# Optimization experiments

Hardware: AMD Instinct MI355X
Metric: run time of the kernel (lower is better)

Reference implementation:

```python
import jax, jax.numpy as jnp
import numpy as np

N = 100000        # num nodes
F_IN = 256        # params['topo_feature']
C = 128           # params['num_edge'] (hidden & GCN channels)
E = 1_600_000     # num edges (avg degree 16)


def setup_inputs() -> dict:
    key = jax.random.key(0)
    k = jax.random.split(key, 6)
    x = jax.random.normal(k[0], (N, F_IN), dtype=jnp.float32)
    edge_index = jax.random.randint(k[1], (2, E), 0, N, dtype=jnp.int32)
    # fc1: Linear(F_IN, C)
    W1 = jax.random.normal(k[2], (C, F_IN), dtype=jnp.float32) * (1.0 / np.sqrt(F_IN))
    b1 = jnp.zeros((C,), dtype=jnp.float32)
    # GCNConv linear: Linear(C, C, bias=False) weight + separate bias added post-aggregation
    W2 = jax.random.normal(k[3], (C, C), dtype=jnp.float32) * (1.0 / np.sqrt(C))
    b2 = jnp.zeros((C,), dtype=jnp.float32)
    return {"x": x, "edge_index": edge_index, "W1": W1, "b1": b1, "W2": W2, "b2": b2}


def reference(x, edge_index, W1, b1, W2, b2):
    # fc1 + relu
    h = jax.nn.relu(x @ W1.T + b1)                       # [N, C]
    # GCNConv: transform, add self-loops, sym-normalize, scatter-add
    z = h @ W2.T                                         # [N, C]
    loop = jnp.arange(N, dtype=edge_index.dtype)
    src = jnp.concatenate([edge_index[0], loop])         # [E+N]
    dst = jnp.concatenate([edge_index[1], loop])         # [E+N]
    deg = jax.ops.segment_sum(jnp.ones_like(dst, jnp.float32), dst, num_segments=N)
    dinv = jnp.where(deg > 0, jax.lax.rsqrt(jnp.maximum(deg, 1.0)), 0.0)
    norm = (dinv[src] * dinv[dst])[:, None]              # [E+N, 1]
    out = jax.ops.segment_sum(z[src] * norm, dst, num_segments=N) + b2
    return out
```

## Files before the change

kernel.cpp:

```cpp
#include <hip/hip_runtime.h>

typedef unsigned short ushort;
typedef __bf16 bf16x8 __attribute__((ext_vector_type(8)));
typedef float f32x4 __attribute__((ext_vector_type(4)));

#define F_IN 256
#define CCH  128
#define BSH  7
#define BNODES 128
#define NBUCK 1024
#define CHUNK 2048

__device__ __forceinline__ ushort f2bf(float f) {
    union { float f; unsigned i; } u; u.f = f;
    unsigned r = u.i + 0x7fffu + ((u.i >> 16) & 1u);
    return (ushort)(r >> 16);
}
__device__ __forceinline__ float2 bf2f2(unsigned u) {
    union { unsigned i; float f; } lo, hi;
    lo.i = u << 16;
    hi.i = u & 0xffff0000u;
    return make_float2(lo.f, hi.f);
}
__device__ __forceinline__ void gload_lds16(const void* g, void* l) {
    __builtin_amdgcn_global_load_lds((const __attribute__((address_space(1))) unsigned*)g,
                                     (__attribute__((address_space(3))) unsigned*)l, 16, 0, 0);
}

__global__ __launch_bounds__(256)
void hist_cvt(const int* __restrict__ dst, int* __restrict__ histC, int* __restrict__ histT,
              int E, int nchunks, int ncp,
              const float* __restrict__ W1, const float* __restrict__ W2,
              ushort* __restrict__ w1b, ushort* __restrict__ w2b)
{
    const int blk = blockIdx.x, t = threadIdx.x;
    if (blk >= nchunks) {
        int i = (blk - nchunks) * 256 + t;
        if (i < CCH * F_IN) {
            int c  = i & 31;
            int cs = c ^ (((i >> 9) & 3) << 3);
            w1b[(i & ~31) | cs] = f2bf(W1[i]);
        } else {
            int j = i - CCH * F_IN;
            if (j < CCH * CCH) w2b[j] = f2bf(W2[j]);
        }
        return;
    }
    __shared__ int h[NBUCK];
    for (int i = t; i < NBUCK; i += 256) h[i] = 0;
    __syncthreads();
    int cb = blk * CHUNK, ce = min(cb + CHUNK, E);
    for (int e = cb + t; e < ce; e += 256)
        atomicAdd(&h[dst[e] >> BSH], 1);
    __syncthreads();
    for (int i = t; i < NBUCK; i += 256) {
        int v = h[i];
        histC[blk * NBUCK + i] = v;
        histT[i * ncp + blk]   = v;
    }
}

__global__ __launch_bounds__(256)
void scan_buckets(const int* __restrict__ histT, int* __restrict__ prefT,
                  int* __restrict__ btot, int nchunks, int ncp)
{
    const int b = blockIdx.x * 4 + (threadIdx.x >> 6);
    const int lane = threadIdx.x & 63;
    int carry = 0;
    for (int c = 0; c < nchunks; c += 64) {
        int idx = c + lane;
        int v = (idx < nchunks) ? histT[b * ncp + idx] : 0;
        int inc = v;
#pragma unroll
        for (int off = 1; off < 64; off <<= 1) {
            int x = __shfl_up(inc, off, 64);
            if (lane >= off) inc += x;
        }
        if (idx < nchunks) prefT[b * ncp + idx] = carry + inc - v;
        carry += __shfl(inc, 63, 64);
    }
    if (lane == 0) btot[b] = carry;
}

__device__ __forceinline__ void partition_body(unsigned* smem4,
    const int* __restrict__ src, const int* __restrict__ dst,
    const int* __restrict__ histC, const int* __restrict__ prefT,
    const int* __restrict__ btot, int* __restrict__ gbase,
    unsigned* __restrict__ pairs, int E, int ncp, int blk)
{
    int* lbase  = (int*)smem4;
    int* lcur   = lbase + NBUCK;
    int* rb2    = lcur + NBUCK;
    int* base_s = rb2 + NBUCK;
    int* ssum   = base_s + NBUCK;
    unsigned* sp = (unsigned*)(ssum + 256);
    ushort* sb  = (ushort*)(sp + CHUNK);
    const int t = threadIdx.x;

    int4 cv = *(const int4*)&histC[blk * NBUCK + 4 * t];
    int tsum = cv.x + cv.y + cv.z + cv.w;
    ssum[t] = tsum;
    __syncthreads();
    for (int off = 1; off < 256; off <<= 1) {
        int x = (t >= off) ? ssum[t - off] : 0;
        __syncthreads();
        ssum[t] += x;
        __syncthreads();
    }
    int texcl = ssum[t] - tsum;
    lbase[4 * t]     = texcl;
    lbase[4 * t + 1] = texcl + cv.x;
    lbase[4 * t + 2] = texcl + cv.x + cv.y;
    lbase[4 * t + 3] = texcl + cv.x + cv.y + cv.z;
    lcur[4 * t]     = lbase[4 * t];
    lcur[4 * t + 1] = lbase[4 * t + 1];
    lcur[4 * t + 2] = lbase[4 * t + 2];
    lcur[4 * t + 3] = lbase[4 * t + 3];
    __syncthreads();

    int4 bt = *(const int4*)&btot[4 * t];
    int bsum = bt.x + bt.y + bt.z + bt.w;
    ssum[t] = bsum;
    __syncthreads();
    for (int off = 1; off < 256; off <<= 1) {
        int x = (t >= off) ? ssum[t - off] : 0;
        __syncthreads();
        ssum[t] += x;
        __syncthreads();
    }
    int bexcl = ssum[t] - bsum;
    base_s[4 * t]     = bexcl;
    base_s[4 * t + 1] = bexcl + bt.x;
    base_s[4 * t + 2] = bexcl + bt.x + bt.y;
    base_s[4 * t + 3] = bexcl + bt.x + bt.y + bt.z;
    if (blk == 0) {
        *(int4*)&gbase[4 * t] = *(int4*)&base_s[4 * t];
        if (t == 255) gbase[NBUCK] = ssum[255];
    }
    __syncthreads();
    for (int i = t; i < NBUCK; i += 256)
        rb2[i] = base_s[i] + prefT[i * ncp + blk];
    __syncthreads();

    const int cb = blk * CHUNK, ce = min(cb + CHUNK, E);
    for (int e = cb + t; e < ce; e += 256) {
        int d = dst[e];
        int b = d >> BSH;
        unsigned packed = ((unsigned)src[e] << BSH) | (unsigned)(d & (BNODES - 1));
        int p = atomicAdd(&lcur[b], 1);
        sp[p] = packed;
        sb[p] = (ushort)b;
    }
    __syncthreads();
    const int cnt = ce - cb;
    for (int i = t; i < cnt; i += 256) {
        int b = sb[i];
        pairs[rb2[b] + (i - lbase[b])] = sp[i];
    }
}

__device__ __forceinline__ void csr_body(unsigned* smem4,
    const unsigned* __restrict__ pairs, const int* __restrict__ base,
    int* __restrict__ row_start, float* __restrict__ dinv,
    unsigned* __restrict__ csr, int N, int E, int b, int lastb)
{
    int* deg = (int*)smem4;
    int* s   = deg + BNODES;
    int* cur = s + BNODES;
    const int t = threadIdx.x;
    if (t < BNODES) deg[t] = 0;
    __syncthreads();
    const int rb = base[b], re = base[b + 1];
    for (int e = rb + t; e < re; e += 256)
        atomicAdd(&deg[pairs[e] & (BNODES - 1)], 1);
    __syncthreads();
    int v = (t < BNODES) ? deg[t] : 0;
    if (t < BNODES) s[t] = v;
    __syncthreads();
    for (int off = 1; off < BNODES; off <<= 1) {
        int x = (t >= off && t < BNODES) ? s[t - off] : 0;
        __syncthreads();
        if (t < BNODES) s[t] += x;
        __syncthreads();
    }
    const int n0 = b << BSH;
    if (t < BNODES) {
        int excl = s[t] - v;
        cur[t] = excl;
        if (n0 + t < N) {
            row_start[n0 + t] = rb + excl;
            dinv[n0 + t] = rsqrtf((float)v + 1.0f);
        }
    }
    if (b == lastb && t == 0) row_start[N] = E;
    __syncthreads();
    for (int e = rb + t; e < re; e += 256) {
        unsigned p = pairs[e];
        int l = p & (BNODES - 1);
        int slot = atomicAdd(&cur[l], 1);
        csr[rb + slot] = p >> BSH;
    }
}

__device__ __forceinline__ void gemm_body(unsigned* smem4,
    const float* __restrict__ X, const ushort* __restrict__ W1b,
    const ushort* __restrict__ W2b, const float* __restrict__ b1,
    ushort* __restrict__ Zq, int M, int m0)
{
    ushort* smem = (ushort*)smem4;
    ushort* Ht = smem;
    const int tid  = threadIdx.x;
    const int wave = tid >> 6, lane = tid & 63;
    const int wm = (wave & 1) * 64, wn = (wave >> 1) * 64;
    const int lr = lane & 15, lq = lane >> 4;

    const int arow = tid >> 2;
    const int aq   = tid & 3;

    float4 ar[2][2];
    auto loadX = [&](int k0) {
#pragma unroll
        for (int it = 0; it < 2; it++) {
            int row = arow + it * 64;
            ar[it][0] = make_float4(0.f, 0.f, 0.f, 0.f);
            ar[it][1] = make_float4(0.f, 0.f, 0.f, 0.f);
            if (m0 + row < M) {
                const float* p = &X[(long)(m0 + row) * F_IN + k0 + aq * 8];
                ar[it][0] = *(const float4*)p;
                ar[it][1] = *(const float4*)(p + 4);
            }
        }
    };
    auto writeA = [&](ushort* As) {
#pragma unroll
        for (int it = 0; it < 2; it++) {
            int row = arow + it * 64;
            ushort u[8] = { f2bf(ar[it][0].x), f2bf(ar[it][0].y), f2bf(ar[it][0].z), f2bf(ar[it][0].w),
                            f2bf(ar[it][1].x), f2bf(ar[it][1].y), f2bf(ar[it][1].z), f2bf(ar[it][1].w) };
            *(uint4*)&As[row * 32 + ((aq ^ ((row >> 1) & 3)) << 3)] = *(uint4*)u;
        }
    };
    auto stageB = [&](int k0, ushort* Bs) {
#pragma unroll
        for (int it = 0; it < 2; it++) {
            int r0 = wave * 32 + it * 16;
            const ushort* g = &W1b[(long)(r0 + (lane >> 2)) * F_IN + k0 + (lane & 3) * 8];
            gload_lds16(g, &Bs[r0 * 32]);
        }
    };

    f32x4 acc[4][4] = {};
    loadX(0);
    stageB(0, smem + 4096);
    writeA(smem);
    __syncthreads();
    for (int k0 = 0; k0 < F_IN; k0 += 32) {
        const int cur = (k0 >> 5) & 1;
        ushort* As = smem + cur * 8192;
        ushort* Bs = As + 4096;
        const bool more = (k0 + 32 < F_IN);
        if (more) {
            stageB(k0 + 32, smem + (cur ^ 1) * 8192 + 4096);
            loadX(k0 + 32);
        }
        bf16x8 af[4], bfr[4];
#pragma unroll
        for (int t4 = 0; t4 < 4; t4++) {
            int ra = wm + t4 * 16 + lr;
            int rb = wn + t4 * 16 + lr;
            af[t4]  = *(bf16x8*)&As[ra * 32 + ((lq ^ ((ra >> 1) & 3)) << 3)];
            bfr[t4] = *(bf16x8*)&Bs[rb * 32 + ((lq ^ ((rb >> 1) & 3)) << 3)];
        }
#pragma unroll
        for (int i = 0; i < 4; i++)
#pragma unroll
            for (int j = 0; j < 4; j++)
                acc[i][j] = __builtin_amdgcn_mfma_f32_16x16x32_bf16(af[i], bfr[j], acc[i][j], 0, 0, 0);
        if (more) writeA(smem + (cur ^ 1) * 8192);
        __syncthreads();
    }

    uint4 wb[2][4];
#pragma unroll
    for (int t4 = 0; t4 < 4; t4++)
        wb[0][t4] = *(const uint4*)&W2b[(long)(wn + t4 * 16 + lr) * CCH + lq * 8];

    {
        float bv[4];
#pragma unroll
        for (int j = 0; j < 4; j++) bv[j] = b1[wn + j * 16 + lr];
#pragma unroll
        for (int i = 0; i < 4; i++)
#pragma unroll
            for (int r = 0; r < 4; r++) {
                int row = wm + i * 16 + lq * 4 + r;
                int rx  = (row & 7) << 3;
#pragma unroll
                for (int j = 0; j < 4; j++)
                    Ht[row * 128 + ((wn + j * 16 + lr) ^ rx)] = f2bf(fmaxf(acc[i][j][r] + bv[j], 0.f));
            }
    }
    __syncthreads();

    f32x4 acc2[4][4] = {};
#pragma unroll
    for (int kk = 0; kk < 4; kk++) {
        const int k0 = kk * 32;
        if (kk < 3) {
#pragma unroll
            for (int t4 = 0; t4 < 4; t4++)
                wb[(kk + 1) & 1][t4] =
                    *(const uint4*)&W2b[(long)(wn + t4 * 16 + lr) * CCH + k0 + 32 + lq * 8];
        }
        bf16x8 af[4];
#pragma unroll
        for (int t4 = 0; t4 < 4; t4++) {
            int ra = wm + t4 * 16 + lr;
            af[t4] = *(bf16x8*)&Ht[ra * 128 + ((k0 + lq * 8) ^ ((ra & 7) << 3))];
        }
#pragma unroll
        for (int i = 0; i < 4; i++)
#pragma unroll
            for (int j = 0; j < 4; j++)
                acc2[i][j] = __builtin_amdgcn_mfma_f32_16x16x32_bf16(af[i], *(bf16x8*)&wb[kk & 1][j],
                                                                     acc2[i][j], 0, 0, 0);
    }
    __syncthreads();

#pragma unroll
    for (int i = 0; i < 4; i++)
#pragma unroll
        for (int r = 0; r < 4; r++) {
            int row = wm + i * 16 + lq * 4 + r;
            int rx  = (row & 7) << 3;
#pragma unroll
            for (int j = 0; j < 4; j++)
                Ht[row * 128 + ((wn + j * 16 + lr) ^ rx)] = f2bf(acc2[i][j][r]);
        }
    __syncthreads();
    {
        int colq = tid & 15, row0 = tid >> 4;
#pragma unroll
        for (int i = 0; i < 8; i++) {
            int row = row0 + i * 16;
            if (m0 + row < M)
                *(uint4*)&Zq[(long)(m0 + row) * CCH + colq * 8] =
                    *(uint4*)&Ht[row * 128 + ((colq * 8) ^ ((row & 7) << 3))];
        }
    }
}

__global__ __launch_bounds__(256)
void u_part_gemm(const int* __restrict__ src, const int* __restrict__ dst,
                 const int* __restrict__ histC, const int* __restrict__ prefT,
                 const int* __restrict__ btot, int* __restrict__ gbase,
                 unsigned* __restrict__ pairs, int E, int ncp, int ngA,
                 const float* __restrict__ X, const ushort* __restrict__ W1b,
                 const ushort* __restrict__ W2b, const float* __restrict__ b1,
                 ushort* __restrict__ Zq, int M)
{
    __shared__ unsigned smem4[8192];
    if ((int)blockIdx.x < ngA)
        gemm_body(smem4, X, W1b, W2b, b1, Zq, M, blockIdx.x * 128);
    else
        partition_body(smem4, src, dst, histC, prefT, btot, gbase, pairs, E, ncp,
                       blockIdx.x - ngA);
}

__global__ __launch_bounds__(256)
void u_csr_gemm(const unsigned* __restrict__ pairs, const int* __restrict__ base,
                int* __restrict__ row_start, float* __restrict__ dinv,
                unsigned* __restrict__ csr, int N, int E, int ngB, int ngA, int nbuck,
                const float* __restrict__ X, const ushort* __restrict__ W1b,
                const ushort* __restrict__ W2b, const float* __restrict__ b1,
                ushort* __restrict__ Zq, int M)
{
    __shared__ unsigned smem4[8192];
    if ((int)blockIdx.x < ngB)
        gemm_body(smem4, X, W1b, W2b, b1, Zq, M, (ngA + blockIdx.x) * 128);
    else
        csr_body(smem4, pairs, base, row_start, dinv, csr, N, E,
                 blockIdx.x - ngB, nbuck - 1);
}

__global__ __launch_bounds__(256)
void gather_nodes(const unsigned* __restrict__ zq, const unsigned* __restrict__ csr,
                  const int* __restrict__ row_start, const float* __restrict__ dinv,
                  const float* __restrict__ b2, float* __restrict__ out, int N)
{
    const int node = blockIdx.x * 4 + (threadIdx.x >> 6);
    const int lane = threadIdx.x & 63;
    if (node >= N) return;

    const float di = dinv[node];
    float2 zs = bf2f2(zq[(long)node * 64 + lane]);
    float acc0 = di * zs.x, acc1 = di * zs.y;

    const int rs = row_start[node];
    const int re = row_start[node + 1];
    int j = rs;
    for (; j + 8 <= re; j += 8) {
        unsigned sI[8], zv[8];
        float dv[8];
#pragma unroll
        for (int q = 0; q < 8; q++) sI[q] = csr[j + q];
#pragma unroll
        for (int q = 0; q < 8; q++) dv[q] = dinv[sI[q]];
#pragma unroll
        for (int q = 0; q < 8; q++) zv[q] = zq[(long)sI[q] * 64 + lane];
#pragma unroll
        for (int q = 0; q < 8; q++) { float2 f = bf2f2(zv[q]); acc0 += dv[q] * f.x; acc1 += dv[q] * f.y; }
    }
    for (; j < re; j++) {
        unsigned s = csr[j];
        float ds = dinv[s];
        float2 f = bf2f2(zq[(long)s * 64 + lane]);
        acc0 += ds * f.x; acc1 += ds * f.y;
    }

    float2 o;
    o.x = b2[lane * 2 + 0] + di * acc0;
    o.y = b2[lane * 2 + 1] + di * acc1;
    *(float2*)&out[(long)node * CCH + lane * 2] = o;
}

extern "C" void kernel_launch(void* const* d_in, const int* in_sizes, int n_in,
                              void* d_out, int out_size, void* d_ws, size_t ws_size,
                              hipStream_t stream)
{
    const float* x  = (const float*)d_in[0];
    const int*   ei = (const int*)d_in[1];
    const float* W1 = (const float*)d_in[2];
    const float* b1 = (const float*)d_in[3];
    const float* W2 = (const float*)d_in[4];
    const float* b2 = (const float*)d_in[5];
    float* out = (float*)d_out;

    const int N = in_sizes[0] / F_IN;
    const int E = in_sizes[1] / 2;
    const int* src = ei;
    const int* dst = ei + E;

    const int nchunks = (E + CHUNK - 1) / CHUNK;
    const int ncp     = (nchunks + 63) & ~63;
    const int nbuck   = (N + BNODES - 1) / BNODES;
    const int ngrid   = (N + 127) / 128;
    const int ngA     = (ngrid + 1) / 2;
    const int ngB     = ngrid - ngA;
    const int ncvt    = (CCH * F_IN + CCH * CCH + 255) / 256;

    char* ws = (char*)d_ws;
    ushort* zq    = (ushort*)ws;   ws += (size_t)N * CCH * 2;
    ushort* w1b   = (ushort*)ws;   ws += (size_t)CCH * F_IN * 2;
    ushort* w2b   = (ushort*)ws;   ws += (size_t)CCH * CCH * 2;
    unsigned* prs = (unsigned*)ws; ws += (size_t)E * 4;
    unsigned* csr = (unsigned*)ws; ws += (size_t)E * 4;
    int* rstart   = (int*)ws;      ws += ((size_t)N + 1) * 4;
    float* dinv   = (float*)ws;    ws += (size_t)N * 4;
    int* histC    = (int*)ws;      ws += (size_t)nchunks * NBUCK * 4;
    int* histT    = (int*)ws;      ws += (size_t)NBUCK * ncp * 4;
    int* prefT    = (int*)ws;      ws += (size_t)NBUCK * ncp * 4;
    int* btot     = (int*)ws;      ws += NBUCK * 4;
    int* gbase    = (int*)ws;      ws += (NBUCK + 1) * 4;

    hist_cvt<<<nchunks + ncvt, 256, 0, stream>>>(dst, histC, histT, E, nchunks, ncp, W1, W2, w1b, w2b);
    scan_buckets<<<NBUCK / 4, 256, 0, stream>>>(histT, prefT, btot, nchunks, ncp);
    u_part_gemm<<<ngA + nchunks, 256, 0, stream>>>(src, dst, histC, prefT, btot, gbase, prs, E, ncp,
                                                   ngA, x, w1b, w2b, b1, zq, N);
    u_csr_gemm<<<ngB + nbuck, 256, 0, stream>>>(prs, gbase, rstart, dinv, csr, N, E,
                                                ngB, ngA, nbuck, x, w1b, w2b, b1, zq, N);
    gather_nodes<<<(N + 3) / 4, 256, 0, stream>>>((const unsigned*)zq, csr, rstart, dinv, b2, out, N);
}
```

Measured before the change: 318.8 us.

## Split GEMM across three fused launches to overlap with histogram stage

Weight conversion becomes its own small kernel, and the histogram stage is fused with a third of the GEMM tiles. The remaining GEMM tiles are split between the partition and CSR kernels. This spreads the dense GEMM over three graph-build phases so the irregular histogram work no longer runs alone. It adds one extra launch. The X loads also drop the bounds branch and clamp the row index instead, which reads duplicate rows at the tail.

```diff
diff --git a/kernel.cpp b/kernel.cpp
--- a/kernel.cpp
+++ b/kernel.cpp
@@ -28,25 +28,26 @@
 }
 
 __global__ __launch_bounds__(256)
-void hist_cvt(const int* __restrict__ dst, int* __restrict__ histC, int* __restrict__ histT,
-              int E, int nchunks, int ncp,
-              const float* __restrict__ W1, const float* __restrict__ W2,
-              ushort* __restrict__ w1b, ushort* __restrict__ w2b)
-{
-    const int blk = blockIdx.x, t = threadIdx.x;
-    if (blk >= nchunks) {
-        int i = (blk - nchunks) * 256 + t;
-        if (i < CCH * F_IN) {
-            int c  = i & 31;
-            int cs = c ^ (((i >> 9) & 3) << 3);
-            w1b[(i & ~31) | cs] = f2bf(W1[i]);
-        } else {
-            int j = i - CCH * F_IN;
-            if (j < CCH * CCH) w2b[j] = f2bf(W2[j]);
-        }
-        return;
-    }
-    __shared__ int h[NBUCK];
+void cvt_w(const float* __restrict__ W1, const float* __restrict__ W2,
+           ushort* __restrict__ w1b, ushort* __restrict__ w2b)
+{
+    int i = blockIdx.x * 256 + threadIdx.x;
+    if (i < CCH * F_IN) {
+        int c  = i & 31;
+        int cs = c ^ (((i >> 9) & 3) << 3);
+        w1b[(i & ~31) | cs] = f2bf(W1[i]);
+    } else {
+        int j = i - CCH * F_IN;
+        if (j < CCH * CCH) w2b[j] = f2bf(W2[j]);
+    }
+}
+
+__device__ __forceinline__ void hist_body(unsigned* smem4,
+    const int* __restrict__ dst, int* __restrict__ histC, int* __restrict__ histT,
+    int E, int ncp, int blk)
+{
+    int* h = (int*)smem4;
+    const int t = threadIdx.x;
     for (int i = t; i < NBUCK; i += 256) h[i] = 0;
     __syncthreads();
     int cb = blk * CHUNK, ce = min(cb + CHUNK, E);
@@ -221,14 +222,10 @@
     auto loadX = [&](int k0) {
 #pragma unroll
         for (int it = 0; it < 2; it++) {
-            int row = arow + it * 64;
-            ar[it][0] = make_float4(0.f, 0.f, 0.f, 0.f);
-            ar[it][1] = make_float4(0.f, 0.f, 0.f, 0.f);
-            if (m0 + row < M) {
-                const float* p = &X[(long)(m0 + row) * F_IN + k0 + aq * 8];
-                ar[it][0] = *(const float4*)p;
-                ar[it][1] = *(const float4*)(p + 4);
-            }
+            int grow = min(m0 + arow + it * 64, M - 1);
+            const float* p = &X[(long)grow * F_IN + k0 + aq * 8];
+            ar[it][0] = *(const float4*)p;
+            ar[it][1] = *(const float4*)(p + 4);
         }
     };
     auto writeA = [&](ushort* As) {
@@ -351,36 +348,50 @@
 }
 
 __global__ __launch_bounds__(256)
-void u_part_gemm(const int* __restrict__ src, const int* __restrict__ dst,
-                 const int* __restrict__ histC, const int* __restrict__ prefT,
-                 const int* __restrict__ btot, int* __restrict__ gbase,
-                 unsigned* __restrict__ pairs, int E, int ncp, int ngA,
-                 const float* __restrict__ X, const ushort* __restrict__ W1b,
+void u_gemm_hist(const float* __restrict__ X, const ushort* __restrict__ W1b,
                  const ushort* __restrict__ W2b, const float* __restrict__ b1,
-                 ushort* __restrict__ Zq, int M)
+                 ushort* __restrict__ Zq, int M, int ngA,
+                 const int* __restrict__ dst, int* __restrict__ histC,
+                 int* __restrict__ histT, int E, int ncp)
 {
     __shared__ unsigned smem4[8192];
     if ((int)blockIdx.x < ngA)
         gemm_body(smem4, X, W1b, W2b, b1, Zq, M, blockIdx.x * 128);
     else
-        partition_body(smem4, src, dst, histC, prefT, btot, gbase, pairs, E, ncp,
-                       blockIdx.x - ngA);
-}
-
-__global__ __launch_bounds__(256)
-void u_csr_gemm(const unsigned* __restrict__ pairs, const int* __restrict__ base,
-                int* __restrict__ row_start, float* __restrict__ dinv,
-                unsigned* __restrict__ csr, int N, int E, int ngB, int ngA, int nbuck,
-                const float* __restrict__ X, const ushort* __restrict__ W1b,
-                const ushort* __restrict__ W2b, const float* __restrict__ b1,
-                ushort* __restrict__ Zq, int M)
+        hist_body(smem4, dst, histC, histT, E, ncp, blockIdx.x - ngA);
+}
+
+__global__ __launch_bounds__(256)
+void u_gemm_part(const int* __restrict__ src, const int* __restrict__ dst,
+                 const int* __restrict__ histC, const int* __restrict__ prefT,
+                 const int* __restrict__ btot, int* __restrict__ gbase,
+                 unsigned* __restrict__ pairs, int E, int ncp, int ngA, int ngB,
+                 const float* __restrict__ X, const ushort* __restrict__ W1b,
+                 const ushort* __restrict__ W2b, const float* __restrict__ b1,
+                 ushort* __restrict__ Zq, int M)
 {
     __shared__ unsigned smem4[8192];
     if ((int)blockIdx.x < ngB)
         gemm_body(smem4, X, W1b, W2b, b1, Zq, M, (ngA + blockIdx.x) * 128);
     else
+        partition_body(smem4, src, dst, histC, prefT, btot, gbase, pairs, E, ncp,
+                       blockIdx.x - ngB);
+}
+
+__global__ __launch_bounds__(256)
+void u_gemm_csr(const unsigned* __restrict__ pairs, const int* __restrict__ base,
+                int* __restrict__ row_start, float* __restrict__ dinv,
+                unsigned* __restrict__ csr, int N, int E, int ngAB, int ngC, int nbuck,
+                const float* __restrict__ X, const ushort* __restrict__ W1b,
+                const ushort* __restrict__ W2b, const float* __restrict__ b1,
+                ushort* __restrict__ Zq, int M)
+{
+    __shared__ unsigned smem4[8192];
+    if ((int)blockIdx.x < ngC)
+        gemm_body(smem4, X, W1b, W2b, b1, Zq, M, (ngAB + blockIdx.x) * 128);
+    else
         csr_body(smem4, pairs, base, row_start, dinv, csr, N, E,
-                 blockIdx.x - ngB, nbuck - 1);
+                 blockIdx.x - ngC, nbuck - 1);
 }
 
 __global__ __launch_bounds__(256)
@@ -445,8 +456,9 @@
     const int ncp     = (nchunks + 63) & ~63;
     const int nbuck   = (N + BNODES - 1) / BNODES;
     const int ngrid   = (N + 127) / 128;
-    const int ngA     = (ngrid + 1) / 2;
-    const int ngB     = ngrid - ngA;
+    const int ngA     = (ngrid + 2) / 3;
+    const int ngB     = (ngrid - ngA + 1) / 2;
+    const int ngC     = ngrid - ngA - ngB;
     const int ncvt    = (CCH * F_IN + CCH * CCH + 255) / 256;
 
     char* ws = (char*)d_ws;
@@ -463,11 +475,13 @@
     int* btot     = (int*)ws;      ws += NBUCK * 4;
     int* gbase    = (int*)ws;      ws += (NBUCK + 1) * 4;
 
-    hist_cvt<<<nchunks + ncvt, 256, 0, stream>>>(dst, histC, histT, E, nchunks, ncp, W1, W2, w1b, w2b);
+    cvt_w<<<ncvt, 256, 0, stream>>>(W1, W2, w1b, w2b);
+    u_gemm_hist<<<ngA + nchunks, 256, 0, stream>>>(x, w1b, w2b, b1, zq, N, ngA,
+                                                   dst, histC, histT, E, ncp);
     scan_buckets<<<NBUCK / 4, 256, 0, stream>>>(histT, prefT, btot, nchunks, ncp);
-    u_part_gemm<<<ngA + nchunks, 256, 0, stream>>>(src, dst, histC, prefT, btot, gbase, prs, E, ncp,
-                                                   ngA, x, w1b, w2b, b1, zq, N);
-    u_csr_gemm<<<ngB + nbuck, 256, 0, stream>>>(prs, gbase, rstart, dinv, csr, N, E,
-                                                ngB, ngA, nbuck, x, w1b, w2b, b1, zq, N);
+    u_gemm_part<<<ngB + nchunks, 256, 0, stream>>>(src, dst, histC, prefT, btot, gbase, prs,
+                                                   E, ncp, ngA, ngB, x, w1b, w2b, b1, zq, N);
+    u_gemm_csr<<<ngC + nbuck, 256, 0, stream>>>(prs, gbase, rstart, dinv, csr, N, E,
+                                                ngA + ngB, ngC, nbuck, x, w1b, w2b, b1, zq, N);
     gather_nodes<<<(N + 3) / 4, 256, 0, stream>>>((const unsigned*)zq, csr, rstart, dinv, b2, out, N);
 }
```

After: 327.5 us. 2.7% more time.

## Reorder fused partition/GEMM blocks, XCD-aware chunk mapping, tiled histogram transpose

Applied to the files above, without the earlier changes.

Partition and CSR blocks are now dispatched before the GEMM blocks in the two fused kernels, so the latency-critical graph work starts first and the GEMM fills in behind it. Partition chunks are remapped so that each of the 8 round-robin dispatch slots (XCDs) handles a contiguous range of chunks. The transposed histogram is stored in 16-bucket tiles so that both hist_cvt writes and scan reads touch contiguous 64B segments. The GEMM X loads also clamp the row index instead of branching, which removes divergence at the cost of redundantly loading the last row for tail tiles.

```diff
diff --git a/kernel.cpp b/kernel.cpp
--- a/kernel.cpp
+++ b/kernel.cpp
@@ -53,10 +53,11 @@
     for (int e = cb + t; e < ce; e += 256)
         atomicAdd(&h[dst[e] >> BSH], 1);
     __syncthreads();
+    const int ncp16 = ncp * 16;
     for (int i = t; i < NBUCK; i += 256) {
         int v = h[i];
         histC[blk * NBUCK + i] = v;
-        histT[i * ncp + blk]   = v;
+        histT[(i >> 4) * ncp16 + blk * 16 + (i & 15)] = v;
     }
 }
 
@@ -66,10 +67,11 @@
 {
     const int b = blockIdx.x * 4 + (threadIdx.x >> 6);
     const int lane = threadIdx.x & 63;
+    const int tbase = (b >> 4) * (ncp * 16) + (b & 15);
     int carry = 0;
     for (int c = 0; c < nchunks; c += 64) {
         int idx = c + lane;
-        int v = (idx < nchunks) ? histT[b * ncp + idx] : 0;
+        int v = (idx < nchunks) ? histT[tbase + idx * 16] : 0;
         int inc = v;
 #pragma unroll
         for (int off = 1; off < 64; off <<= 1) {
@@ -221,14 +223,10 @@
     auto loadX = [&](int k0) {
 #pragma unroll
         for (int it = 0; it < 2; it++) {
-            int row = arow + it * 64;
-            ar[it][0] = make_float4(0.f, 0.f, 0.f, 0.f);
-            ar[it][1] = make_float4(0.f, 0.f, 0.f, 0.f);
-            if (m0 + row < M) {
-                const float* p = &X[(long)(m0 + row) * F_IN + k0 + aq * 8];
-                ar[it][0] = *(const float4*)p;
-                ar[it][1] = *(const float4*)(p + 4);
-            }
+            int grow = min(m0 + arow + it * 64, M - 1);
+            const float* p = &X[(long)grow * F_IN + k0 + aq * 8];
+            ar[it][0] = *(const float4*)p;
+            ar[it][1] = *(const float4*)(p + 4);
         }
     };
     auto writeA = [&](ushort* As) {
@@ -354,33 +352,37 @@
 void u_part_gemm(const int* __restrict__ src, const int* __restrict__ dst,
                  const int* __restrict__ histC, const int* __restrict__ prefT,
                  const int* __restrict__ btot, int* __restrict__ gbase,
-                 unsigned* __restrict__ pairs, int E, int ncp, int ngA,
+                 unsigned* __restrict__ pairs, int E, int ncp, int nchunks,
                  const float* __restrict__ X, const ushort* __restrict__ W1b,
                  const ushort* __restrict__ W2b, const float* __restrict__ b1,
                  ushort* __restrict__ Zq, int M)
 {
     __shared__ unsigned smem4[8192];
-    if ((int)blockIdx.x < ngA)
-        gemm_body(smem4, X, W1b, W2b, b1, Zq, M, blockIdx.x * 128);
-    else
-        partition_body(smem4, src, dst, histC, prefT, btot, gbase, pairs, E, ncp,
-                       blockIdx.x - ngA);
+    const int bid = blockIdx.x;
+    if (bid < nchunks) {
+        const int x = bid & 7, i = bid >> 3;
+        const int q = nchunks >> 3, r = nchunks & 7;
+        const int chunk = (x < r) ? x * (q + 1) + i : r * (q + 1) + (x - r) * q + i;
+        partition_body(smem4, src, dst, histC, prefT, btot, gbase, pairs, E, ncp, chunk);
+    } else {
+        gemm_body(smem4, X, W1b, W2b, b1, Zq, M, (bid - nchunks) * 128);
+    }
 }
 
 __global__ __launch_bounds__(256)
 void u_csr_gemm(const unsigned* __restrict__ pairs, const int* __restrict__ base,
                 int* __restrict__ row_start, float* __restrict__ dinv,
-                unsigned* __restrict__ csr, int N, int E, int ngB, int ngA, int nbuck,
+                unsigned* __restrict__ csr, int N, int E, int nbuck, int ngA,
                 const float* __restrict__ X, const ushort* __restrict__ W1b,
                 const ushort* __restrict__ W2b, const float* __restrict__ b1,
                 ushort* __restrict__ Zq, int M)
 {
     __shared__ unsigned smem4[8192];
-    if ((int)blockIdx.x < ngB)
-        gemm_body(smem4, X, W1b, W2b, b1, Zq, M, (ngA + blockIdx.x) * 128);
+    const int bid = blockIdx.x;
+    if (bid < nbuck)
+        csr_body(smem4, pairs, base, row_start, dinv, csr, N, E, bid, nbuck - 1);
     else
-        csr_body(smem4, pairs, base, row_start, dinv, csr, N, E,
-                 blockIdx.x - ngB, nbuck - 1);
+        gemm_body(smem4, X, W1b, W2b, b1, Zq, M, (ngA + bid - nbuck) * 128);
 }
 
 __global__ __launch_bounds__(256)
@@ -465,9 +467,9 @@
 
     hist_cvt<<<nchunks + ncvt, 256, 0, stream>>>(dst, histC, histT, E, nchunks, ncp, W1, W2, w1b, w2b);
     scan_buckets<<<NBUCK / 4, 256, 0, stream>>>(histT, prefT, btot, nchunks, ncp);
-    u_part_gemm<<<ngA + nchunks, 256, 0, stream>>>(src, dst, histC, prefT, btot, gbase, prs, E, ncp,
-                                                   ngA, x, w1b, w2b, b1, zq, N);
-    u_csr_gemm<<<ngB + nbuck, 256, 0, stream>>>(prs, gbase, rstart, dinv, csr, N, E,
-                                                ngB, ngA, nbuck, x, w1b, w2b, b1, zq, N);
+    u_part_gemm<<<nchunks + ngA, 256, 0, stream>>>(src, dst, histC, prefT, btot, gbase, prs,
+                                                   E, ncp, nchunks, x, w1b, w2b, b1, zq, N);
+    u_csr_gemm<<<nbuck + ngB, 256, 0, stream>>>(prs, gbase, rstart, dinv, csr, N, E,
+                                                nbuck, ngA, x, w1b, w2b, b1, zq, N);
     gather_nodes<<<(N + 3) / 4, 256, 0, stream>>>((const unsigned*)zq, csr, rstart, dinv, b2, out, N);
 }
```

New measurement: 314.5 us. No clear change (-1.4%).
